# Optimization experiments

Measured on AMD Instinct MI355X. Metric: run time of the kernel, lower is better.

## Reference

```python
import jax, jax.numpy as jnp
import numpy as np

N, C, H, W = 8, 256, 128, 128
HW = H * W
NB = 20            # boxes per image
TEMP = 0.5
RATIO = 1.0
IMG_H, IMG_W = 800.0, 800.0  # img_metas[i]['img_shape']


def setup_inputs() -> dict:
    key = jax.random.key(0)
    k1, k2, k3 = jax.random.split(key, 3)
    preds_S = jax.random.normal(k1, (HW, N, C), dtype=jnp.float32)
    preds_T = jax.random.normal(k2, (HW, N, C), dtype=jnp.float32)
    # boxes: random corner pairs in image coords, sorted so x1<=x2, y1<=y2
    u = jax.random.uniform(k3, (N, NB, 4), dtype=jnp.float32)
    x1 = jnp.minimum(u[..., 0], u[..., 2]) * IMG_W
    x2 = jnp.maximum(u[..., 0], u[..., 2]) * IMG_W
    y1 = jnp.minimum(u[..., 1], u[..., 3]) * IMG_H
    y2 = jnp.maximum(u[..., 1], u[..., 3]) * IMG_H
    gt_bboxes = jnp.stack([x1, y1, x2, y2], axis=-1)  # (N, NB, 4)
    return {"preds_S": preds_S, "preds_T": preds_T, "gt_bboxes": gt_bboxes}


def get_attention(preds, temp):
    # preds: (N, C, H, W)
    value = jnp.abs(preds)
    fea_map = value.mean(axis=1)                                   # (N, H, W)
    S_att = (H * W) * jax.nn.softmax((fea_map / temp).reshape(N, -1), axis=1)
    S_att = S_att.reshape(N, H, W)
    channel_map = value.mean(axis=(2, 3))                          # (N, C)
    C_att = C * jax.nn.softmax(channel_map / temp, axis=1)
    return S_att, C_att


def build_masks(gt_bboxes):
    # boxes scaled to feature grid (same math as torch loop, vectorized)
    wmin = jnp.floor(gt_bboxes[..., 0] / IMG_W * W).astype(jnp.int32)  # (N, NB)
    wmax = jnp.ceil(gt_bboxes[..., 2] / IMG_W * W).astype(jnp.int32)
    hmin = jnp.floor(gt_bboxes[..., 1] / IMG_H * H).astype(jnp.int32)
    hmax = jnp.ceil(gt_bboxes[..., 3] / IMG_H * H).astype(jnp.int32)
    area = 1.0 / (hmax + 1 - hmin).astype(jnp.float32) / (wmax + 1 - wmin).astype(jnp.float32)
    hh = jnp.arange(H)[None, None, :, None]
    ww = jnp.arange(W)[None, None, None, :]
    inside = ((hh >= hmin[:, :, None, None]) & (hh <= hmax[:, :, None, None]) &
              (ww >= wmin[:, :, None, None]) & (ww <= wmax[:, :, None, None]))  # (N, NB, H, W)
    # per-box max-scatter == max over boxes of (area where inside else 0)
    Mask_fg = jnp.max(jnp.where(inside, area[:, :, None, None], 0.0), axis=1)  # (N, H, W)
    Mask_bg = (Mask_fg <= 0).astype(jnp.float32)
    s = Mask_bg.sum(axis=(1, 2), keepdims=True)
    Mask_bg = jnp.where(s > 0, Mask_bg / s, Mask_bg)
    return Mask_fg, Mask_bg


def reference(preds_S, preds_T, gt_bboxes):
    # attention from DETACHED teacher features (preds_T.detach() in torch)
    pT_det = jax.lax.stop_gradient(preds_T)
    pT_new = pT_det.reshape(H, W, N, C).transpose(2, 3, 0, 1)  # (N, C, H, W)
    S_t, C_t = get_attention(pT_new, TEMP)

    Mask_fg, Mask_bg = build_masks(gt_bboxes)

    # flatten to the (HW, bs, .) layout of get_fea_loss
    flat = lambda m: m.transpose(1, 2, 0).reshape(HW, N, 1)
    S_t_f = flat(S_t)
    Mfg_f = flat(Mask_fg)
    Mbg_f = flat(Mask_bg)
    C_t_f = C_t[None]  # (1, bs, c) broadcast

    w = jnp.sqrt(S_t_f) * jnp.sqrt(C_t_f)
    fea_t = preds_T * w
    fea_s = preds_S * w
    diff = jnp.abs(fea_s - fea_t)
    fg_loss = jnp.sum(diff * jnp.sqrt(Mfg_f)) / HW
    bg_loss = jnp.sum(diff * jnp.sqrt(Mbg_f)) / HW
    return (fg_loss + bg_loss) * RATIO
```

## Files before the change

kernel.cpp:

```cpp
#include <hip/hip_runtime.h>

#define N_   8
#define C_   256
#define H_   128
#define W_   128
#define HW_  16384
#define NB_  20
constexpr float TEMP  = 0.5f;
constexpr float IMG_W = 800.0f;
constexpr float IMG_H = 800.0f;

typedef float f32x4 __attribute__((ext_vector_type(4)));

__global__ __launch_bounds__(256) void k_stats(const float* __restrict__ pT,
                                               float* __restrict__ chan_part,
                                               float* __restrict__ fea_sum) {
    const int n    = blockIdx.x & 7;
    const int p    = blockIdx.x >> 3;
    const int wave = threadIdx.x >> 6;
    const int lane = threadIdx.x & 63;
    __shared__ float rowp[4][64 * 65];
    __shared__ float chl[4][C_];

    float4 cacc = make_float4(0.f, 0.f, 0.f, 0.f);
    const int hw0 = p * 256 + wave * 64;
    const float* base = pT + ((size_t)(hw0 * N_ + n)) * C_ + lane * 4;
    #pragma unroll 8
    for (int i = 0; i < 64; ++i) {
        const float4 v = *(const float4*)(base + (size_t)i * (N_ * C_));
        const float ax = fabsf(v.x), ay = fabsf(v.y), az = fabsf(v.z), aw = fabsf(v.w);
        cacc.x += ax; cacc.y += ay; cacc.z += az; cacc.w += aw;
        rowp[wave][i * 65 + lane] = ax + ay + az + aw;
    }
    chl[wave][lane * 4 + 0] = cacc.x;
    chl[wave][lane * 4 + 1] = cacc.y;
    chl[wave][lane * 4 + 2] = cacc.z;
    chl[wave][lane * 4 + 3] = cacc.w;
    __syncthreads();
    {
        const int w_ = threadIdx.x >> 6, r = threadIdx.x & 63;
        float s = 0.f;
        #pragma unroll
        for (int j = 0; j < 64; ++j) s += rowp[w_][r * 65 + j];
        fea_sum[n * HW_ + p * 256 + threadIdx.x] = s;
    }
    const int c = threadIdx.x;
    chan_part[((size_t)(n * 64 + p)) * C_ + c] =
        chl[0][c] + chl[1][c] + chl[2][c] + chl[3][c];
}

__global__ __launch_bounds__(256) void k_perN(const float* __restrict__ fea_sum,
                                              const float* __restrict__ chan_part,
                                              const float* __restrict__ gt,
                                              float* __restrict__ A,
                                              float* __restrict__ B) {
    const int n = blockIdx.x;
    const int tid = threadIdx.x;
    __shared__ float red[256];
    __shared__ int   bh0[NB_], bh1[NB_], bw0[NB_], bw1[NB_];
    __shared__ float barea[NB_];
    __shared__ float MfgL[HW_];
    __shared__ float sc[1];

    if (tid < NB_) {
        const float* bx = gt + ((size_t)n * NB_ + tid) * 4;
        const float wminf = floorf(bx[0] / IMG_W * (float)W_);
        const float wmaxf = ceilf (bx[2] / IMG_W * (float)W_);
        const float hminf = floorf(bx[1] / IMG_H * (float)H_);
        const float hmaxf = ceilf (bx[3] / IMG_H * (float)H_);
        bw0[tid] = (int)wminf; bw1[tid] = (int)wmaxf;
        bh0[tid] = (int)hminf; bh1[tid] = (int)hmaxf;
        barea[tid] = 1.0f / (hmaxf + 1.0f - hminf) / (wmaxf + 1.0f - wminf);
    }

    float csum = 0.f;
    for (int p = 0; p < 64; ++p)
        csum += chan_part[((size_t)(n * 64 + p)) * C_ + tid];
    const float lc = csum * (1.0f / (HW_ * TEMP));
    red[tid] = lc; __syncthreads();
    for (int s = 128; s > 0; s >>= 1) { if (tid < s) red[tid] = fmaxf(red[tid], red[tid + s]); __syncthreads(); }
    const float cmax = red[0]; __syncthreads();
    const float e = expf(lc - cmax);
    red[tid] = e; __syncthreads();
    for (int s = 128; s > 0; s >>= 1) { if (tid < s) red[tid] += red[tid + s]; __syncthreads(); }
    if (tid == 0) sc[0] = red[0];
    __syncthreads();
    B[n * C_ + tid] = sqrtf((float)C_ * e / sc[0]);

    __syncthreads();
    float m = -1e30f;
    for (int i = tid; i < HW_; i += 256) m = fmaxf(m, fea_sum[n * HW_ + i]);
    red[tid] = m; __syncthreads();
    for (int s = 128; s > 0; s >>= 1) { if (tid < s) red[tid] = fmaxf(red[tid], red[tid + s]); __syncthreads(); }
    const float smax = red[0] * (1.0f / (C_ * TEMP));
    __syncthreads();
    float acc = 0.f;
    for (int i = tid; i < HW_; i += 256)
        acc += expf(fea_sum[n * HW_ + i] * (1.0f / (C_ * TEMP)) - smax);
    red[tid] = acc; __syncthreads();
    for (int s = 128; s > 0; s >>= 1) { if (tid < s) red[tid] += red[tid + s]; __syncthreads(); }
    const float sden = red[0];
    __syncthreads();

    const int w = tid & 127;
    unsigned wmask = 0;
    for (int b = 0; b < NB_; ++b)
        if (w >= bw0[b] && w <= bw1[b]) wmask |= (1u << b);
    float cnt = 0.f;
    for (int k = 0; k < HW_ / 256; ++k) {
        const int i = tid + k * 256;
        const int h = i >> 7;
        float fg = 0.f;
        for (int b = 0; b < NB_; ++b)
            if (((wmask >> b) & 1u) && h >= bh0[b] && h <= bh1[b]) fg = fmaxf(fg, barea[b]);
        MfgL[i] = fg;
        cnt += (fg <= 0.f) ? 1.f : 0.f;
    }
    red[tid] = cnt; __syncthreads();
    for (int s = 128; s > 0; s >>= 1) { if (tid < s) red[tid] += red[tid + s]; __syncthreads(); }
    const float bgsum = red[0];
    const float bgval = (bgsum > 0.f) ? 1.0f / bgsum : 1.0f;

    for (int k = 0; k < HW_ / 256; ++k) {
        const int i = tid + k * 256;
        const float fg = MfgL[i];
        const float S_att = (float)HW_ *
            expf(fea_sum[n * HW_ + i] * (1.0f / (C_ * TEMP)) - smax) / sden;
        const float bgv = (fg <= 0.f) ? bgval : 0.f;
        A[n * HW_ + i] = sqrtf(S_att) * (sqrtf(fg) + sqrtf(bgv)) * (1.0f / (float)HW_);
    }
}

__device__ __forceinline__ float waveReduceSum(float v) {
    v += __shfl_xor(v, 32, 64);
    v += __shfl_xor(v, 16, 64);
    v += __shfl_xor(v, 8, 64);
    v += __shfl_xor(v, 4, 64);
    v += __shfl_xor(v, 2, 64);
    v += __shfl_xor(v, 1, 64);
    return v;
}

__global__ __launch_bounds__(256) void k_main(const float* __restrict__ pS,
                                              const float* __restrict__ pT,
                                              const float* __restrict__ A,
                                              const float* __restrict__ B,
                                              float* __restrict__ partials) {
    const int wave = threadIdx.x >> 6, lane = threadIdx.x & 63;
    const int wg = blockIdx.x * 4 + wave;
    const int n = wg & 7;
    const int widx = wg >> 3;
    const float4 B4 = *(const float4*)(B + n * C_ + lane * 4);
    float acc = 0.f;
    const int hw0 = widx * 32;
    #pragma unroll 4
    for (int i = 0; i < 32; ++i) {
        const int hw = hw0 + i;
        const size_t off = ((size_t)(hw * N_ + n)) * C_ + lane * 4;
        const float4 tv = *(const float4*)(pT + off);
        const f32x4  sv = __builtin_nontemporal_load((const f32x4*)(pS + off));
        const float part = fabsf(sv.x - tv.x) * B4.x + fabsf(sv.y - tv.y) * B4.y +
                           fabsf(sv.z - tv.z) * B4.z + fabsf(sv.w - tv.w) * B4.w;
        acc += A[n * HW_ + hw] * part;
    }
    acc = waveReduceSum(acc);
    __shared__ float red[4];
    if (lane == 0) red[wave] = acc;
    __syncthreads();
    if (threadIdx.x == 0) partials[blockIdx.x] = red[0] + red[1] + red[2] + red[3];
}

__global__ __launch_bounds__(256) void k_final(const float* __restrict__ partials,
                                               float* __restrict__ out) {
    float a = 0.f;
    for (int i = threadIdx.x; i < 1024; i += 256) a += partials[i];
    __shared__ float red[256];
    red[threadIdx.x] = a; __syncthreads();
    for (int s = 128; s > 0; s >>= 1) { if (threadIdx.x < s) red[threadIdx.x] += red[threadIdx.x + s]; __syncthreads(); }
    if (threadIdx.x == 0) out[0] = red[0];
}

extern "C" void kernel_launch(void* const* d_in, const int* in_sizes, int n_in,
                              void* d_out, int out_size, void* d_ws, size_t ws_size,
                              hipStream_t stream) {
    const float* pS = (const float*)d_in[0];
    const float* pT = (const float*)d_in[1];
    const float* gt = (const float*)d_in[2];
    float* ws = (float*)d_ws;

    float* chan_part = ws;
    float* fea_sum   = ws + 131072;
    float* A         = fea_sum + N_ * HW_;
    float* B         = A + N_ * HW_;
    float* partials  = B + N_ * C_;

    k_stats<<<512, 256, 0, stream>>>(pT, chan_part, fea_sum);
    k_perN<<<N_, 256, 0, stream>>>(fea_sum, chan_part, gt, A, B);
    k_main<<<1024, 256, 0, stream>>>(pS, pT, A, B, partials);
    k_final<<<1, 256, 0, stream>>>(partials, (float*)d_out);
}
```

Measured before the change: 344.5 us.

## Compute fp16 abs-diff in stats pass and reduce it in the main pass

The stats kernel now reads both student and teacher features and writes |S−T| as fp16 into workspace. The main reduction kernel then reads only this half-size diff buffer instead of both fp32 inputs. Total DRAM traffic stays about the same: two full reads move earlier and a smaller write plus read are added. The aim is to shorten the second pass and let the diff buffer stay in the last-level cache. The fp16 storage of the differences adds rounding error to the loss.

```diff
diff --git a/kernel.cpp b/kernel.cpp
--- a/kernel.cpp
+++ b/kernel.cpp
@@ -10,11 +10,14 @@
 constexpr float IMG_W = 800.0f;
 constexpr float IMG_H = 800.0f;
 
-typedef float f32x4 __attribute__((ext_vector_type(4)));
-
-__global__ __launch_bounds__(256) void k_stats(const float* __restrict__ pT,
-                                               float* __restrict__ chan_part,
-                                               float* __restrict__ fea_sum) {
+typedef float    f32x4 __attribute__((ext_vector_type(4)));
+typedef _Float16 f16x4 __attribute__((ext_vector_type(4)));
+
+__global__ __launch_bounds__(256) void k_statsD(const float* __restrict__ pS,
+                                                const float* __restrict__ pT,
+                                                _Float16* __restrict__ D,
+                                                float* __restrict__ chan_part,
+                                                float* __restrict__ fea_sum) {
     const int n    = blockIdx.x & 7;
     const int p    = blockIdx.x >> 3;
     const int wave = threadIdx.x >> 6;
@@ -24,13 +27,21 @@
 
     float4 cacc = make_float4(0.f, 0.f, 0.f, 0.f);
     const int hw0 = p * 256 + wave * 64;
-    const float* base = pT + ((size_t)(hw0 * N_ + n)) * C_ + lane * 4;
-    #pragma unroll 8
+    const size_t base = ((size_t)(hw0 * N_ + n)) * C_ + lane * 4;
+    #pragma unroll 4
     for (int i = 0; i < 64; ++i) {
-        const float4 v = *(const float4*)(base + (size_t)i * (N_ * C_));
-        const float ax = fabsf(v.x), ay = fabsf(v.y), az = fabsf(v.z), aw = fabsf(v.w);
+        const size_t off = base + (size_t)i * (N_ * C_);
+        const f32x4 tv = __builtin_nontemporal_load((const f32x4*)(pT + off));
+        const f32x4 sv = __builtin_nontemporal_load((const f32x4*)(pS + off));
+        const float ax = fabsf(tv.x), ay = fabsf(tv.y), az = fabsf(tv.z), aw = fabsf(tv.w);
         cacc.x += ax; cacc.y += ay; cacc.z += az; cacc.w += aw;
         rowp[wave][i * 65 + lane] = ax + ay + az + aw;
+        f16x4 d;
+        d.x = (_Float16)fabsf(sv.x - tv.x);
+        d.y = (_Float16)fabsf(sv.y - tv.y);
+        d.z = (_Float16)fabsf(sv.z - tv.z);
+        d.w = (_Float16)fabsf(sv.w - tv.w);
+        *(f16x4*)(D + off) = d;
     }
     chl[wave][lane * 4 + 0] = cacc.x;
     chl[wave][lane * 4 + 1] = cacc.y;
@@ -141,11 +152,10 @@
     return v;
 }
 
-__global__ __launch_bounds__(256) void k_main(const float* __restrict__ pS,
-                                              const float* __restrict__ pT,
-                                              const float* __restrict__ A,
-                                              const float* __restrict__ B,
-                                              float* __restrict__ partials) {
+__global__ __launch_bounds__(256) void k_red(const _Float16* __restrict__ D,
+                                             const float* __restrict__ A,
+                                             const float* __restrict__ B,
+                                             float* __restrict__ partials) {
     const int wave = threadIdx.x >> 6, lane = threadIdx.x & 63;
     const int wg = blockIdx.x * 4 + wave;
     const int n = wg & 7;
@@ -153,14 +163,13 @@
     const float4 B4 = *(const float4*)(B + n * C_ + lane * 4);
     float acc = 0.f;
     const int hw0 = widx * 32;
-    #pragma unroll 4
+    #pragma unroll 8
     for (int i = 0; i < 32; ++i) {
         const int hw = hw0 + i;
         const size_t off = ((size_t)(hw * N_ + n)) * C_ + lane * 4;
-        const float4 tv = *(const float4*)(pT + off);
-        const f32x4  sv = __builtin_nontemporal_load((const f32x4*)(pS + off));
-        const float part = fabsf(sv.x - tv.x) * B4.x + fabsf(sv.y - tv.y) * B4.y +
-                           fabsf(sv.z - tv.z) * B4.z + fabsf(sv.w - tv.w) * B4.w;
+        const f16x4 dv = *(const f16x4*)(D + off);
+        const float part = (float)dv.x * B4.x + (float)dv.y * B4.y +
+                           (float)dv.z * B4.z + (float)dv.w * B4.w;
         acc += A[n * HW_ + hw] * part;
     }
     acc = waveReduceSum(acc);
@@ -188,14 +197,15 @@
     const float* gt = (const float*)d_in[2];
     float* ws = (float*)d_ws;
 
-    float* chan_part = ws;
-    float* fea_sum   = ws + 131072;
-    float* A         = fea_sum + N_ * HW_;
-    float* B         = A + N_ * HW_;
-    float* partials  = B + N_ * C_;
-
-    k_stats<<<512, 256, 0, stream>>>(pT, chan_part, fea_sum);
+    float*    chan_part = ws;
+    float*    fea_sum   = ws + 131072;
+    float*    A         = fea_sum + N_ * HW_;
+    float*    B         = A + N_ * HW_;
+    float*    partials  = B + N_ * C_;
+    _Float16* D         = (_Float16*)(partials + 1024);
+
+    k_statsD<<<512, 256, 0, stream>>>(pS, pT, D, chan_part, fea_sum);
     k_perN<<<N_, 256, 0, stream>>>(fea_sum, chan_part, gt, A, B);
-    k_main<<<1024, 256, 0, stream>>>(pS, pT, A, B, partials);
+    k_red<<<1024, 256, 0, stream>>>(D, A, B, partials);
     k_final<<<1, 256, 0, stream>>>(partials, (float*)d_out);
 }
```

Measured after the change: 344.1 us. No clear change (-0.1%).
